# Performance work log

Hardware: AMD Instinct MI355X
Metric: run time of the kernel (lower is better)

The kernel has to match this reference:

```python
import jax, jax.numpy as jnp
import numpy as np

S, B, D = 2048, 8, 2048


def setup_inputs() -> dict:
    key = jax.random.key(0)
    ks = jax.random.split(key, 10)
    scale = 1.0 / np.sqrt(D)
    return {
        "x": jax.random.normal(ks[0], (S, B, D), dtype=jnp.float32),
        "layer_input": jax.random.normal(ks[1], (S, B, D), dtype=jnp.float32),
        "position_embedding": jax.random.normal(ks[2], (S, B, D), dtype=jnp.float32),
        "encoder_padding_mask": jnp.zeros((B, S), dtype=bool),
        "langs": jnp.zeros((B,), dtype=jnp.int64),
        "W1": jax.random.uniform(ks[3], (D, D), jnp.float32, -scale, scale),
        "b1": jax.random.uniform(ks[4], (D,), jnp.float32, -scale, scale),
        "W2": jax.random.uniform(ks[5], (D, D), jnp.float32, -scale, scale),
        "b2": jax.random.uniform(ks[6], (D,), jnp.float32, -scale, scale),
        "V": jax.random.uniform(ks[7], (D, D), jnp.float32, -scale, scale),
        "bV": jax.random.uniform(ks[8], (D,), jnp.float32, -scale, scale),
    }


def reference(x, layer_input, position_embedding, encoder_padding_mask, langs,
              W1, b1, W2, b2, V, bV):
    # Uniform-language path of LSReorderingLayer -> ReorderingLayer (LA_reorder=False).
    # x, layer_input, position_embedding: (S, B, D)
    # position_penalty = tanh(W1(layer_input) + W2(x))
    pp = jnp.tanh(jnp.einsum('sbd,ed->sbe', layer_input, W1) + b1
                  + jnp.einsum('sbd,ed->sbe', x, W2) + b2)
    # position_penalty = sigmoid(V(pp)); reordering = penalty * position_embedding
    gate = jax.nn.sigmoid(jnp.einsum('sbd,ed->sbe', pp, V) + bV)
    return gate * position_embedding
```

## Files before the change

kernel.cpp:

```cpp
#include <hip/hip_runtime.h>
#include <hip/hip_bf16.h>
#include <cstdint>
#include <cstddef>

typedef unsigned short u16;
typedef short short8 __attribute__((ext_vector_type(8)));
typedef float floatx4 __attribute__((ext_vector_type(4)));

#define BM 128
#define BN 128
#define BK 32
#define D_DIM 2048

__device__ __forceinline__ void async_ld16(const u16* g, u16* l) {
  __builtin_amdgcn_global_load_lds(
      (const __attribute__((address_space(1))) void*)g,
      (__attribute__((address_space(3))) void*)l, 16, 0, 0);
}

__device__ __forceinline__ u16 f2bf(float f) {
  __hip_bfloat16 h = __float2bfloat16(f);
  return *reinterpret_cast<u16*>(&h);
}

__device__ __forceinline__ short8 pack8(float4 a, float4 b) {
  short8 p;
  p[0] = (short)f2bf(a.x); p[1] = (short)f2bf(a.y);
  p[2] = (short)f2bf(a.z); p[3] = (short)f2bf(a.w);
  p[4] = (short)f2bf(b.x); p[5] = (short)f2bf(b.y);
  p[6] = (short)f2bf(b.z); p[7] = (short)f2bf(b.w);
  return p;
}

__global__ __launch_bounds__(256) void cvt_f32_bf16(
    const float* __restrict__ src, u16* __restrict__ dst, int n8) {
  int i = blockIdx.x * blockDim.x + threadIdx.x;
  if (i < n8) {
    const float4* s = (const float4*)src + 2 * (size_t)i;
    float4 f0 = s[0], f1 = s[1];
    *((short8*)dst + i) = pack8(f0, f1);
  }
}

__device__ __forceinline__ void phase_f32A(
    const float* __restrict__ A, const u16* __restrict__ Bw,
    int mBase, int nBase, u16* As, u16* Bs, floatx4 acc[4][4])
{
  const int tid  = threadIdx.x;
  const int lane = tid & 63;
  const int quad = lane >> 4;
  const int lrow = lane & 15;
  const int wv   = tid >> 6;
  const int wm   = wv & 1;
  const int wn   = wv >> 1;

  const int r0 = tid >> 2;
  const int c0 = (tid & 3) * 8;
  const u16* gB = Bw + (size_t)(nBase + r0) * D_DIM + c0;
  u16* lB0 = Bs + tid * 8;
  u16* lB1 = Bs + (tid + 256) * 8;

  const int ar = tid >> 1;
  const int ac = (tid & 1) * 16;
  const float* gA = A + (size_t)(mBase + ar) * D_DIM + ac;
  u16* wA = As + ar * BK + ac;

  for (int kt = 0; kt < D_DIM / BK; ++kt) {
    const int k0 = kt * BK;
    __syncthreads();
    async_ld16(gB + k0, lB0);
    async_ld16(gB + (size_t)64 * D_DIM + k0, lB1);
    float4 f0 = *(const float4*)(gA + k0);
    float4 f1 = *(const float4*)(gA + k0 + 4);
    float4 f2 = *(const float4*)(gA + k0 + 8);
    float4 f3 = *(const float4*)(gA + k0 + 12);
    *(short8*)(wA)     = pack8(f0, f1);
    *(short8*)(wA + 8) = pack8(f2, f3);
    __syncthreads();

    short8 a[4], b[4];
#pragma unroll
    for (int i = 0; i < 4; ++i) {
      const int row = wm * 64 + i * 16 + lrow;
      a[i] = *(const short8*)(As + row * BK + quad * 8);
      const int col = wn * 64 + i * 16 + lrow;
      b[i] = *(const short8*)(Bs + col * BK + quad * 8);
    }
#pragma unroll
    for (int i = 0; i < 4; ++i)
#pragma unroll
      for (int j = 0; j < 4; ++j)
        acc[i][j] = __builtin_amdgcn_mfma_f32_16x16x32_bf16(a[i], b[j], acc[i][j], 0, 0, 0);
  }
}

__device__ __forceinline__ void phase_bf16(
    const u16* __restrict__ A, const u16* __restrict__ Bw,
    int mBase, int nBase, u16* As, u16* Bs, floatx4 acc[4][4])
{
  const int tid  = threadIdx.x;
  const int lane = tid & 63;
  const int quad = lane >> 4;
  const int lrow = lane & 15;
  const int wv   = tid >> 6;
  const int wm   = wv & 1;
  const int wn   = wv >> 1;

  const int r0 = tid >> 2;
  const int c0 = (tid & 3) * 8;
  const u16* gA = A + (size_t)(mBase + r0) * D_DIM + c0;
  const u16* gB = Bw + (size_t)(nBase + r0) * D_DIM + c0;
  u16* lA0 = As + tid * 8;
  u16* lA1 = As + (tid + 256) * 8;
  u16* lB0 = Bs + tid * 8;
  u16* lB1 = Bs + (tid + 256) * 8;

  for (int kt = 0; kt < D_DIM / BK; ++kt) {
    const int k0 = kt * BK;
    __syncthreads();
    async_ld16(gA + k0, lA0);
    async_ld16(gA + (size_t)64 * D_DIM + k0, lA1);
    async_ld16(gB + k0, lB0);
    async_ld16(gB + (size_t)64 * D_DIM + k0, lB1);
    __syncthreads();

    short8 a[4], b[4];
#pragma unroll
    for (int i = 0; i < 4; ++i) {
      const int row = wm * 64 + i * 16 + lrow;
      a[i] = *(const short8*)(As + row * BK + quad * 8);
      const int col = wn * 64 + i * 16 + lrow;
      b[i] = *(const short8*)(Bs + col * BK + quad * 8);
    }
#pragma unroll
    for (int i = 0; i < 4; ++i)
#pragma unroll
      for (int j = 0; j < 4; ++j)
        acc[i][j] = __builtin_amdgcn_mfma_f32_16x16x32_bf16(a[i], b[j], acc[i][j], 0, 0, 0);
  }
}

__global__ __launch_bounds__(256) void gemm_pp_kernel(
    const float* __restrict__ li, const float* __restrict__ x,
    const u16* __restrict__ w1b, const u16* __restrict__ w2b,
    const float* __restrict__ b1, const float* __restrict__ b2,
    u16* __restrict__ pp)
{
  __shared__ __align__(16) u16 As[BM * BK];
  __shared__ __align__(16) u16 Bs[BN * BK];

  floatx4 acc[4][4];
#pragma unroll
  for (int i = 0; i < 4; ++i)
#pragma unroll
    for (int j = 0; j < 4; ++j)
      acc[i][j] = (floatx4){0.f, 0.f, 0.f, 0.f};

  const int nBase = blockIdx.x * BN;
  const int mBase = blockIdx.y * BM;

  phase_f32A(li, w1b, mBase, nBase, As, Bs, acc);
  phase_f32A(x,  w2b, mBase, nBase, As, Bs, acc);

  const int tid  = threadIdx.x;
  const int lane = tid & 63;
  const int quad = lane >> 4;
  const int lrow = lane & 15;
  const int wv   = tid >> 6;
  const int wm   = wv & 1;
  const int wn   = wv >> 1;

#pragma unroll
  for (int j = 0; j < 4; ++j) {
    const int col = nBase + wn * 64 + j * 16 + lrow;
    const float bs = b1[col] + b2[col];
#pragma unroll
    for (int i = 0; i < 4; ++i) {
      const int rowb = mBase + wm * 64 + i * 16 + quad * 4;
#pragma unroll
      for (int r = 0; r < 4; ++r) {
        const float v = tanhf(acc[i][j][r] + bs);
        pp[(size_t)(rowb + r) * D_DIM + col] = f2bf(v);
      }
    }
  }
}

__global__ __launch_bounds__(256) void gemm_out_kernel(
    const u16* __restrict__ pp, const u16* __restrict__ vb,
    const float* __restrict__ bV, const float* __restrict__ pe,
    float* __restrict__ out)
{
  __shared__ __align__(16) u16 As[BM * BK];
  __shared__ __align__(16) u16 Bs[BN * BK];

  floatx4 acc[4][4];
#pragma unroll
  for (int i = 0; i < 4; ++i)
#pragma unroll
    for (int j = 0; j < 4; ++j)
      acc[i][j] = (floatx4){0.f, 0.f, 0.f, 0.f};

  const int nBase = blockIdx.x * BN;
  const int mBase = blockIdx.y * BM;

  phase_bf16(pp, vb, mBase, nBase, As, Bs, acc);

  const int tid  = threadIdx.x;
  const int lane = tid & 63;
  const int quad = lane >> 4;
  const int lrow = lane & 15;
  const int wv   = tid >> 6;
  const int wm   = wv & 1;
  const int wn   = wv >> 1;

#pragma unroll
  for (int j = 0; j < 4; ++j) {
    const int col = nBase + wn * 64 + j * 16 + lrow;
    const float bs = bV[col];
#pragma unroll
    for (int i = 0; i < 4; ++i) {
      const int rowb = mBase + wm * 64 + i * 16 + quad * 4;
#pragma unroll
      for (int r = 0; r < 4; ++r) {
        const size_t idx = (size_t)(rowb + r) * D_DIM + col;
        const float t = acc[i][j][r] + bs;
        const float g = 1.f / (1.f + expf(-t));
        out[idx] = g * pe[idx];
      }
    }
  }
}

extern "C" void kernel_launch(void* const* d_in, const int* in_sizes, int n_in,
                              void* d_out, int out_size, void* d_ws, size_t ws_size,
                              hipStream_t stream) {
  const float* x  = (const float*)d_in[0];
  const float* li = (const float*)d_in[1];
  const float* pe = (const float*)d_in[2];
  const float* W1 = (const float*)d_in[5];
  const float* b1 = (const float*)d_in[6];
  const float* W2 = (const float*)d_in[7];
  const float* b2 = (const float*)d_in[8];
  const float* V  = (const float*)d_in[9];
  const float* bV = (const float*)d_in[10];
  float* out = (float*)d_out;

  u16* w1b = (u16*)d_ws;
  u16* w2b = w1b + (size_t)D_DIM * D_DIM;
  u16* vb  = w2b + (size_t)D_DIM * D_DIM;
  u16* pp  = vb  + (size_t)D_DIM * D_DIM;

  const int M = 2048 * 8;
  const int nW8 = (D_DIM * D_DIM) / 8;

  cvt_f32_bf16<<<nW8 / 256, 256, 0, stream>>>(W1, w1b, nW8);
  cvt_f32_bf16<<<nW8 / 256, 256, 0, stream>>>(W2, w2b, nW8);
  cvt_f32_bf16<<<nW8 / 256, 256, 0, stream>>>(V,  vb,  nW8);

  dim3 grid(D_DIM / BN, M / BM);
  dim3 block(256);
  gemm_pp_kernel<<<grid, block, 0, stream>>>(li, x, w1b, w2b, b1, b2, pp);
  gemm_out_kernel<<<grid, block, 0, stream>>>(pp, vb, bV, pe, out);
}
```

Before: 1.115 ms.

## Pre-convert activations to bf16 and swizzle LDS layout in bf16 GEMM path

Adds separate conversion passes that turn layer_input and x into bf16 workspace buffers, so the first GEMM can load both operands with async global-to-LDS copies instead of converting fp32 in registers. This path runs only when the workspace is large enough, otherwise it falls back to the old fp32 kernel. It also applies an XOR swizzle to the LDS column slots in the bf16 phase, aiming to cut bank conflicts in both GEMMs. The cost is extra global traffic to read the fp32 activations and write bf16 copies before the GEMM, plus two more kernel launches.

```diff
diff --git a/kernel.cpp b/kernel.cpp
--- a/kernel.cpp
+++ b/kernel.cpp
@@ -39,6 +39,54 @@
     const float4* s = (const float4*)src + 2 * (size_t)i;
     float4 f0 = s[0], f1 = s[1];
     *((short8*)dst + i) = pack8(f0, f1);
+  }
+}
+
+__device__ __forceinline__ void phase_bf16(
+    const u16* __restrict__ A, const u16* __restrict__ Bw,
+    int mBase, int nBase, u16* As, u16* Bs, floatx4 acc[4][4])
+{
+  const int tid  = threadIdx.x;
+  const int lane = tid & 63;
+  const int quad = lane >> 4;
+  const int lrow = lane & 15;
+  const int wv   = tid >> 6;
+  const int wm   = wv & 1;
+  const int wn   = wv >> 1;
+
+  const int r0 = tid >> 2;
+  const int q0 = (((tid & 3) ^ ((tid >> 3) & 3))) * 8;
+  const u16* gA = A + (size_t)(mBase + r0) * D_DIM + q0;
+  const u16* gB = Bw + (size_t)(nBase + r0) * D_DIM + q0;
+  u16* lA0 = As + tid * 8;
+  u16* lA1 = As + (tid + 256) * 8;
+  u16* lB0 = Bs + tid * 8;
+  u16* lB1 = Bs + (tid + 256) * 8;
+
+  const int slot8 = (quad ^ ((lrow >> 1) & 3)) * 8;
+
+  for (int kt = 0; kt < D_DIM / BK; ++kt) {
+    const int k0 = kt * BK;
+    __syncthreads();
+    async_ld16(gA + k0, lA0);
+    async_ld16(gA + (size_t)64 * D_DIM + k0, lA1);
+    async_ld16(gB + k0, lB0);
+    async_ld16(gB + (size_t)64 * D_DIM + k0, lB1);
+    __syncthreads();
+
+    short8 a[4], b[4];
+#pragma unroll
+    for (int i = 0; i < 4; ++i) {
+      const int row = wm * 64 + i * 16 + lrow;
+      a[i] = *(const short8*)(As + row * BK + slot8);
+      const int col = wn * 64 + i * 16 + lrow;
+      b[i] = *(const short8*)(Bs + col * BK + slot8);
+    }
+#pragma unroll
+    for (int i = 0; i < 4; ++i)
+#pragma unroll
+      for (int j = 0; j < 4; ++j)
+        acc[i][j] = __builtin_amdgcn_mfma_f32_16x16x32_bf16(a[i], b[j], acc[i][j], 0, 0, 0);
   }
 }
 
@@ -94,9 +142,9 @@
   }
 }
 
-__device__ __forceinline__ void phase_bf16(
-    const u16* __restrict__ A, const u16* __restrict__ Bw,
-    int mBase, int nBase, u16* As, u16* Bs, floatx4 acc[4][4])
+__device__ __forceinline__ void epilogue_pp(
+    floatx4 acc[4][4], const float* b1, const float* b2,
+    int mBase, int nBase, u16* pp)
 {
   const int tid  = threadIdx.x;
   const int lane = tid & 63;
@@ -106,70 +154,6 @@
   const int wm   = wv & 1;
   const int wn   = wv >> 1;
 
-  const int r0 = tid >> 2;
-  const int c0 = (tid & 3) * 8;
-  const u16* gA = A + (size_t)(mBase + r0) * D_DIM + c0;
-  const u16* gB = Bw + (size_t)(nBase + r0) * D_DIM + c0;
-  u16* lA0 = As + tid * 8;
-  u16* lA1 = As + (tid + 256) * 8;
-  u16* lB0 = Bs + tid * 8;
-  u16* lB1 = Bs + (tid + 256) * 8;
-
-  for (int kt = 0; kt < D_DIM / BK; ++kt) {
-    const int k0 = kt * BK;
-    __syncthreads();
-    async_ld16(gA + k0, lA0);
-    async_ld16(gA + (size_t)64 * D_DIM + k0, lA1);
-    async_ld16(gB + k0, lB0);
-    async_ld16(gB + (size_t)64 * D_DIM + k0, lB1);
-    __syncthreads();
-
-    short8 a[4], b[4];
-#pragma unroll
-    for (int i = 0; i < 4; ++i) {
-      const int row = wm * 64 + i * 16 + lrow;
-      a[i] = *(const short8*)(As + row * BK + quad * 8);
-      const int col = wn * 64 + i * 16 + lrow;
-      b[i] = *(const short8*)(Bs + col * BK + quad * 8);
-    }
-#pragma unroll
-    for (int i = 0; i < 4; ++i)
-#pragma unroll
-      for (int j = 0; j < 4; ++j)
-        acc[i][j] = __builtin_amdgcn_mfma_f32_16x16x32_bf16(a[i], b[j], acc[i][j], 0, 0, 0);
-  }
-}
-
-__global__ __launch_bounds__(256) void gemm_pp_kernel(
-    const float* __restrict__ li, const float* __restrict__ x,
-    const u16* __restrict__ w1b, const u16* __restrict__ w2b,
-    const float* __restrict__ b1, const float* __restrict__ b2,
-    u16* __restrict__ pp)
-{
-  __shared__ __align__(16) u16 As[BM * BK];
-  __shared__ __align__(16) u16 Bs[BN * BK];
-
-  floatx4 acc[4][4];
-#pragma unroll
-  for (int i = 0; i < 4; ++i)
-#pragma unroll
-    for (int j = 0; j < 4; ++j)
-      acc[i][j] = (floatx4){0.f, 0.f, 0.f, 0.f};
-
-  const int nBase = blockIdx.x * BN;
-  const int mBase = blockIdx.y * BM;
-
-  phase_f32A(li, w1b, mBase, nBase, As, Bs, acc);
-  phase_f32A(x,  w2b, mBase, nBase, As, Bs, acc);
-
-  const int tid  = threadIdx.x;
-  const int lane = tid & 63;
-  const int quad = lane >> 4;
-  const int lrow = lane & 15;
-  const int wv   = tid >> 6;
-  const int wm   = wv & 1;
-  const int wn   = wv >> 1;
-
 #pragma unroll
   for (int j = 0; j < 4; ++j) {
     const int col = nBase + wn * 64 + j * 16 + lrow;
@@ -184,6 +168,54 @@
       }
     }
   }
+}
+
+__global__ __launch_bounds__(256) void gemm_pp_bf16(
+    const u16* __restrict__ lib, const u16* __restrict__ xb,
+    const u16* __restrict__ w1b, const u16* __restrict__ w2b,
+    const float* __restrict__ b1, const float* __restrict__ b2,
+    u16* __restrict__ pp)
+{
+  __shared__ __align__(16) u16 As[BM * BK];
+  __shared__ __align__(16) u16 Bs[BN * BK];
+
+  floatx4 acc[4][4];
+#pragma unroll
+  for (int i = 0; i < 4; ++i)
+#pragma unroll
+    for (int j = 0; j < 4; ++j)
+      acc[i][j] = (floatx4){0.f, 0.f, 0.f, 0.f};
+
+  const int nBase = blockIdx.x * BN;
+  const int mBase = blockIdx.y * BM;
+
+  phase_bf16(lib, w1b, mBase, nBase, As, Bs, acc);
+  phase_bf16(xb,  w2b, mBase, nBase, As, Bs, acc);
+  epilogue_pp(acc, b1, b2, mBase, nBase, pp);
+}
+
+__global__ __launch_bounds__(256) void gemm_pp_f32(
+    const float* __restrict__ li, const float* __restrict__ x,
+    const u16* __restrict__ w1b, const u16* __restrict__ w2b,
+    const float* __restrict__ b1, const float* __restrict__ b2,
+    u16* __restrict__ pp)
+{
+  __shared__ __align__(16) u16 As[BM * BK];
+  __shared__ __align__(16) u16 Bs[BN * BK];
+
+  floatx4 acc[4][4];
+#pragma unroll
+  for (int i = 0; i < 4; ++i)
+#pragma unroll
+    for (int j = 0; j < 4; ++j)
+      acc[i][j] = (floatx4){0.f, 0.f, 0.f, 0.f};
+
+  const int nBase = blockIdx.x * BN;
+  const int mBase = blockIdx.y * BM;
+
+  phase_f32A(li, w1b, mBase, nBase, As, Bs, acc);
+  phase_f32A(x,  w2b, mBase, nBase, As, Bs, acc);
+  epilogue_pp(acc, b1, b2, mBase, nBase, pp);
 }
 
 __global__ __launch_bounds__(256) void gemm_out_kernel(
@@ -246,13 +278,20 @@
   const float* bV = (const float*)d_in[10];
   float* out = (float*)d_out;
 
+  const int M = 2048 * 8;
+  const size_t nW  = (size_t)D_DIM * D_DIM;
+  const size_t nA  = (size_t)M * D_DIM;
+
   u16* w1b = (u16*)d_ws;
-  u16* w2b = w1b + (size_t)D_DIM * D_DIM;
-  u16* vb  = w2b + (size_t)D_DIM * D_DIM;
-  u16* pp  = vb  + (size_t)D_DIM * D_DIM;
-
-  const int M = 2048 * 8;
-  const int nW8 = (D_DIM * D_DIM) / 8;
+  u16* w2b = w1b + nW;
+  u16* vb  = w2b + nW;
+  u16* pp  = vb  + nW;
+  u16* lib = pp  + nA;
+  u16* xb  = lib + nA;
+  const size_t need_full = (3 * nW + 3 * nA) * sizeof(u16);
+
+  const int nW8 = (int)(nW / 8);
+  const int nA8 = (int)(nA / 8);
 
   cvt_f32_bf16<<<nW8 / 256, 256, 0, stream>>>(W1, w1b, nW8);
   cvt_f32_bf16<<<nW8 / 256, 256, 0, stream>>>(W2, w2b, nW8);
@@ -260,6 +299,13 @@
 
   dim3 grid(D_DIM / BN, M / BM);
   dim3 block(256);
-  gemm_pp_kernel<<<grid, block, 0, stream>>>(li, x, w1b, w2b, b1, b2, pp);
+
+  if (ws_size >= need_full) {
+    cvt_f32_bf16<<<nA8 / 256, 256, 0, stream>>>(li, lib, nA8);
+    cvt_f32_bf16<<<nA8 / 256, 256, 0, stream>>>(x,  xb,  nA8);
+    gemm_pp_bf16<<<grid, block, 0, stream>>>(lib, xb, w1b, w2b, b1, b2, pp);
+  } else {
+    gemm_pp_f32<<<grid, block, 0, stream>>>(li, x, w1b, w2b, b1, b2, pp);
+  }
   gemm_out_kernel<<<grid, block, 0, stream>>>(pp, vb, bV, pe, out);
 }
```

Measured after the change: 1.053 ms. 1.06x faster.
